# Optimization experiments

Hardware: AMD Instinct MI355X
Metric: run time of the kernel (lower is better)

The kernel has to match this reference:

```python
import jax, jax.numpy as jnp
import numpy as np

B, L, N = 2048, 64, 1024          # rows, lookback_period, nnodes
E, SE, F, NW, S = 32, 16, 8, 7, 20  # week emb, stop emb, n_features, nweekdays, stops per row
N_SHARED = E + F + SE             # 56; conv kernel width n_f = N_SHARED + 3 = 59


def setup_inputs() -> dict:
    key = jax.random.key(0)
    ks = jax.random.split(key, 12)
    return {
        "x": jax.random.normal(ks[0], (B, L, N), jnp.float32),
        "x_dist": jax.random.normal(ks[1], (N,), jnp.float32),
        "x_features": jax.random.normal(ks[2], (B, F), jnp.float32),
        "x_markov": jax.random.normal(ks[3], (B, N), jnp.float32),
        "stops": jax.random.randint(ks[4], (B, S), 0, N),
        "x_week": jax.random.randint(ks[5], (B,), 0, NW),
        "x_mask": jax.random.randint(ks[6], (B, N), 0, 2, jnp.int32),
        # learned parameters
        "stop_emb": jax.random.normal(ks[7], (N, SE), jnp.float32) * 0.1,
        "week_emb": jax.random.normal(ks[8], (NW, E), jnp.float32) * 0.1,
        "conv_w": jax.random.normal(ks[9], (N, N_SHARED + 3), jnp.float32) * 0.1,  # Conv1d weight [nnodes, 1, n_f] squeezed
        "conv_b": jax.random.normal(ks[10], (N,), jnp.float32) * 0.1,
        "fc1_w": jax.random.normal(ks[11], (L,), jnp.float32) * 0.1,  # Linear(L,1) weight
        "fc1_b": jnp.zeros((), jnp.float32),
    }


def reference(x, x_dist, x_features, x_markov, stops, x_week, x_mask,
              stop_emb, week_emb, conv_w, conv_b, fc1_w, fc1_b):
    # per-row sum of stop embeddings: [B, SE]
    x_embed = stop_emb[stops].sum(axis=1)
    # fc1 over lookback: out[b,n] = sum_l w[l] * x[b,l,n] + b   -> [B, N]
    out = jnp.einsum('bln,l->bn', x, fc1_w) + fc1_b
    # shared (node-independent) features, order matches torch concat: [week_emb, features, stop_emb_sum]
    shared = jnp.concatenate([week_emb[x_week], x_features, x_embed], axis=-1)  # [B, 56]
    # diagonal of strided Conv1d == per-node dot product with that node's kernel
    logits = (shared @ conv_w[:, :N_SHARED].T
              + out * conv_w[:, N_SHARED]
              + x_dist[None, :] * conv_w[:, N_SHARED + 1]
              + x_markov * conv_w[:, N_SHARED + 2]
              + conv_b)  # [B, N]
    logp = jax.nn.log_softmax(logits, axis=1)
    return jnp.where(x_mask.astype(bool), jnp.float32(-1e8), logp)
```

## Files before the change

### kernel.cpp

```cpp
#include <hip/hip_runtime.h>
#include <math.h>

#define BLOCK 256

constexpr int L = 64, N = 1024, E = 32, SE = 16, F = 8, S = 20;
constexpr int NSH = 56;
constexpr int NF  = 59;

typedef float f4 __attribute__((ext_vector_type(4)));

__global__ void prep(const float* __restrict__ x_features,
                     const int*   __restrict__ stops,
                     const int*   __restrict__ x_week,
                     const float* __restrict__ stop_emb,
                     const float* __restrict__ week_emb,
                     const float* __restrict__ conv_w,
                     const float* __restrict__ x_dist,
                     const float* __restrict__ conv_b,
                     float* __restrict__ sh_out,
                     float* __restrict__ w56,
                     float* __restrict__ w58,
                     float* __restrict__ colconst,
                     int B)
{
    const int blk = blockIdx.x;
    const int t = threadIdx.x;
    if (blk < B) {
        const int b = blk;
        if (t < E) {
            sh_out[b * NSH + t] = week_emb[x_week[b] * E + t];
        } else if (t < E + F) {
            sh_out[b * NSH + t] = x_features[b * F + (t - E)];
        } else if (t < NSH) {
            const int j = t - (E + F);
            float s = 0.f;
            #pragma unroll
            for (int k = 0; k < S; ++k)
                s += stop_emb[stops[b * S + k] * SE + j];
            sh_out[b * NSH + t] = s;
        }
    } else {
        const int n = (blk - B) * 64 + t;
        if (n < N) {
            const float* w = conv_w + (size_t)n * NF;
            w56[n] = w[NSH];
            w58[n] = w[NSH + 2];
            colconst[n] = x_dist[n] * w[NSH + 1] + conv_b[n];
        }
    }
}

__global__ __launch_bounds__(BLOCK, 2) void gemm_static(
    const float* __restrict__ shf,
    const float* __restrict__ conv_w,
    const float* __restrict__ colconst,
    float* __restrict__ statc)
{
    __shared__ float Ash[64][NSH + 1];
    __shared__ float Bsh[64][NSH + 1];

    const int n0 = blockIdx.x * 64;
    const int b0 = blockIdx.y * 64;
    const int t  = threadIdx.x;

    for (int idx = t; idx < 64 * NSH; idx += BLOCK) {
        const int r = idx / NSH, c = idx % NSH;
        Ash[r][c] = shf[(size_t)(b0 + r) * NSH + c];
        Bsh[r][c] = conv_w[(size_t)(n0 + r) * NF + c];
    }
    __syncthreads();

    const int tx = t & 15, ty = t >> 4;
    float acc[4][4];
    #pragma unroll
    for (int i = 0; i < 4; ++i)
        #pragma unroll
        for (int k = 0; k < 4; ++k) acc[i][k] = 0.f;

    #pragma unroll 8
    for (int j = 0; j < NSH; ++j) {
        float a[4], bb[4];
        #pragma unroll
        for (int i = 0; i < 4; ++i) a[i]  = Ash[ty * 4 + i][j];
        #pragma unroll
        for (int i = 0; i < 4; ++i) bb[i] = Bsh[tx * 4 + i][j];
        #pragma unroll
        for (int i = 0; i < 4; ++i)
            #pragma unroll
            for (int k = 0; k < 4; ++k)
                acc[i][k] = fmaf(a[i], bb[k], acc[i][k]);
    }

    const float4 cc = *(const float4*)&colconst[n0 + tx * 4];
    #pragma unroll
    for (int i = 0; i < 4; ++i) {
        float4 r;
        r.x = acc[i][0] + cc.x;
        r.y = acc[i][1] + cc.y;
        r.z = acc[i][2] + cc.z;
        r.w = acc[i][3] + cc.w;
        *(float4*)&statc[(size_t)(b0 + ty * 4 + i) * N + n0 + tx * 4] = r;
    }
}

__global__ __launch_bounds__(BLOCK, 4) void markov_main(
    const float* __restrict__ x,
    const float* __restrict__ statc,
    const float* __restrict__ w56,
    const float* __restrict__ w58,
    const float* __restrict__ x_markov,
    const int*   __restrict__ x_mask,
    const float* __restrict__ fc1_w,
    const float* __restrict__ fc1_b,
    float* __restrict__ out)
{
    constexpr int NWAVE = BLOCK / 64;
    __shared__ float sh_fc1[L];
    __shared__ float red_max[NWAVE];
    __shared__ float red_sum[NWAVE];

    const int b = blockIdx.x;
    const int t = threadIdx.x;

    if (t < L) sh_fc1[t] = fc1_w[t];
    __syncthreads();

    const f4* xb = (const f4*)(x + (size_t)b * L * N);
    f4 acc = (f4)(0.f);
    #pragma unroll 16
    for (int l = 0; l < L; ++l) {
        const float w = sh_fc1[l];
        const f4 v = __builtin_nontemporal_load(&xb[l * (N / 4) + t]);
        acc[0] = fmaf(w, v[0], acc[0]);
        acc[1] = fmaf(w, v[1], acc[1]);
        acc[2] = fmaf(w, v[2], acc[2]);
        acc[3] = fmaf(w, v[3], acc[3]);
    }
    const float bias = fc1_b[0];

    const float4 st = ((const float4*)(statc + (size_t)b * N))[t];
    const float4 wa = ((const float4*)w56)[t];
    const float4 wc = ((const float4*)w58)[t];
    const float4 mk = ((const float4*)(x_markov + (size_t)b * N))[t];

    float lg[4];
    lg[0] = st.x + (acc[0] + bias) * wa.x + mk.x * wc.x;
    lg[1] = st.y + (acc[1] + bias) * wa.y + mk.y * wc.y;
    lg[2] = st.z + (acc[2] + bias) * wa.z + mk.z * wc.z;
    lg[3] = st.w + (acc[3] + bias) * wa.w + mk.w * wc.w;

    float lmax = fmaxf(fmaxf(lg[0], lg[1]), fmaxf(lg[2], lg[3]));
    #pragma unroll
    for (int off = 32; off > 0; off >>= 1)
        lmax = fmaxf(lmax, __shfl_down(lmax, off, 64));
    if ((t & 63) == 0) red_max[t >> 6] = lmax;
    __syncthreads();
    float m = red_max[0];
    #pragma unroll
    for (int i = 1; i < NWAVE; ++i) m = fmaxf(m, red_max[i]);

    float se = 0.f;
    #pragma unroll
    for (int i = 0; i < 4; ++i) se += __expf(lg[i] - m);
    #pragma unroll
    for (int off = 32; off > 0; off >>= 1)
        se += __shfl_down(se, off, 64);
    if ((t & 63) == 0) red_sum[t >> 6] = se;
    __syncthreads();
    float Z = 0.f;
    #pragma unroll
    for (int i = 0; i < NWAVE; ++i) Z += red_sum[i];
    const float logZ = m + __logf(Z);

    const int4 mask = ((const int4*)(x_mask + (size_t)b * N))[t];
    f4 res;
    res[0] = mask.x ? -1e8f : (lg[0] - logZ);
    res[1] = mask.y ? -1e8f : (lg[1] - logZ);
    res[2] = mask.z ? -1e8f : (lg[2] - logZ);
    res[3] = mask.w ? -1e8f : (lg[3] - logZ);
    __builtin_nontemporal_store(res, &((f4*)(out + (size_t)b * N))[t]);
}

extern "C" void kernel_launch(void* const* d_in, const int* in_sizes, int n_in,
                              void* d_out, int out_size, void* d_ws, size_t ws_size,
                              hipStream_t stream) {
    const float* x          = (const float*)d_in[0];
    const float* x_dist     = (const float*)d_in[1];
    const float* x_features = (const float*)d_in[2];
    const float* x_markov   = (const float*)d_in[3];
    const int*   stops      = (const int*)  d_in[4];
    const int*   x_week     = (const int*)  d_in[5];
    const int*   x_mask     = (const int*)  d_in[6];
    const float* stop_emb   = (const float*)d_in[7];
    const float* week_emb   = (const float*)d_in[8];
    const float* conv_w     = (const float*)d_in[9];
    const float* conv_b     = (const float*)d_in[10];
    const float* fc1_w      = (const float*)d_in[11];
    const float* fc1_b      = (const float*)d_in[12];
    float* out = (float*)d_out;

    const int B = in_sizes[5];

    char* ws = (char*)d_ws;
    float* sh_f     = (float*)(ws);
    float* w56      = (float*)(ws + ((size_t)B * NSH * 4 + 255) / 256 * 256);
    float* w58      = w56 + N;
    float* colconst = w58 + N;
    float* statc    = (float*)((char*)colconst + ((size_t)N * 4 + 255) / 256 * 256);

    prep<<<B + N / 64, 64, 0, stream>>>(x_features, stops, x_week,
                                        stop_emb, week_emb, conv_w, x_dist, conv_b,
                                        sh_f, w56, w58, colconst, B);
    dim3 ggrid(N / 64, B / 64);
    gemm_static<<<ggrid, BLOCK, 0, stream>>>(sh_f, conv_w, colconst, statc);
    markov_main<<<B, BLOCK, 0, stream>>>(x, statc, w56, w58, x_markov, x_mask,
                                         fc1_w, fc1_b, out);
}
```

Measured before the change: 703.6 us.

## Fuse prep, static GEMM and softmax into one per-row kernel

Replaces the three-kernel pipeline (prep, tiled static GEMM writing a B×N buffer, main softmax kernel) with a single kernel per row. Each block builds the 56 shared features in LDS and computes its row's static logits directly from conv_w in registers. This removes the intermediate statc round-trip through global memory and two launches. The cost is redundant per-block recomputation and strided, uncoalesced conv_w reads across threads.

```diff
diff --git a/kernel.cpp b/kernel.cpp
--- a/kernel.cpp
+++ b/kernel.cpp
@@ -9,121 +9,63 @@
 
 typedef float f4 __attribute__((ext_vector_type(4)));
 
-__global__ void prep(const float* __restrict__ x_features,
-                     const int*   __restrict__ stops,
-                     const int*   __restrict__ x_week,
-                     const float* __restrict__ stop_emb,
-                     const float* __restrict__ week_emb,
-                     const float* __restrict__ conv_w,
-                     const float* __restrict__ x_dist,
-                     const float* __restrict__ conv_b,
-                     float* __restrict__ sh_out,
-                     float* __restrict__ w56,
-                     float* __restrict__ w58,
-                     float* __restrict__ colconst,
-                     int B)
-{
-    const int blk = blockIdx.x;
-    const int t = threadIdx.x;
-    if (blk < B) {
-        const int b = blk;
-        if (t < E) {
-            sh_out[b * NSH + t] = week_emb[x_week[b] * E + t];
-        } else if (t < E + F) {
-            sh_out[b * NSH + t] = x_features[b * F + (t - E)];
-        } else if (t < NSH) {
-            const int j = t - (E + F);
-            float s = 0.f;
-            #pragma unroll
-            for (int k = 0; k < S; ++k)
-                s += stop_emb[stops[b * S + k] * SE + j];
-            sh_out[b * NSH + t] = s;
-        }
-    } else {
-        const int n = (blk - B) * 64 + t;
-        if (n < N) {
-            const float* w = conv_w + (size_t)n * NF;
-            w56[n] = w[NSH];
-            w58[n] = w[NSH + 2];
-            colconst[n] = x_dist[n] * w[NSH + 1] + conv_b[n];
-        }
-    }
-}
-
-__global__ __launch_bounds__(BLOCK, 2) void gemm_static(
-    const float* __restrict__ shf,
+__global__ __launch_bounds__(BLOCK, 4) void fused_markov(
+    const float* __restrict__ x,
+    const float* __restrict__ x_dist,
+    const float* __restrict__ x_features,
+    const float* __restrict__ x_markov,
+    const int*   __restrict__ stops,
+    const int*   __restrict__ x_week,
+    const int*   __restrict__ x_mask,
+    const float* __restrict__ stop_emb,
+    const float* __restrict__ week_emb,
     const float* __restrict__ conv_w,
-    const float* __restrict__ colconst,
-    float* __restrict__ statc)
-{
-    __shared__ float Ash[64][NSH + 1];
-    __shared__ float Bsh[64][NSH + 1];
-
-    const int n0 = blockIdx.x * 64;
-    const int b0 = blockIdx.y * 64;
-    const int t  = threadIdx.x;
-
-    for (int idx = t; idx < 64 * NSH; idx += BLOCK) {
-        const int r = idx / NSH, c = idx % NSH;
-        Ash[r][c] = shf[(size_t)(b0 + r) * NSH + c];
-        Bsh[r][c] = conv_w[(size_t)(n0 + r) * NF + c];
-    }
-    __syncthreads();
-
-    const int tx = t & 15, ty = t >> 4;
-    float acc[4][4];
-    #pragma unroll
-    for (int i = 0; i < 4; ++i)
-        #pragma unroll
-        for (int k = 0; k < 4; ++k) acc[i][k] = 0.f;
-
-    #pragma unroll 8
-    for (int j = 0; j < NSH; ++j) {
-        float a[4], bb[4];
-        #pragma unroll
-        for (int i = 0; i < 4; ++i) a[i]  = Ash[ty * 4 + i][j];
-        #pragma unroll
-        for (int i = 0; i < 4; ++i) bb[i] = Bsh[tx * 4 + i][j];
-        #pragma unroll
-        for (int i = 0; i < 4; ++i)
-            #pragma unroll
-            for (int k = 0; k < 4; ++k)
-                acc[i][k] = fmaf(a[i], bb[k], acc[i][k]);
-    }
-
-    const float4 cc = *(const float4*)&colconst[n0 + tx * 4];
-    #pragma unroll
-    for (int i = 0; i < 4; ++i) {
-        float4 r;
-        r.x = acc[i][0] + cc.x;
-        r.y = acc[i][1] + cc.y;
-        r.z = acc[i][2] + cc.z;
-        r.w = acc[i][3] + cc.w;
-        *(float4*)&statc[(size_t)(b0 + ty * 4 + i) * N + n0 + tx * 4] = r;
-    }
-}
-
-__global__ __launch_bounds__(BLOCK, 4) void markov_main(
-    const float* __restrict__ x,
-    const float* __restrict__ statc,
-    const float* __restrict__ w56,
-    const float* __restrict__ w58,
-    const float* __restrict__ x_markov,
-    const int*   __restrict__ x_mask,
+    const float* __restrict__ conv_b,
     const float* __restrict__ fc1_w,
     const float* __restrict__ fc1_b,
     float* __restrict__ out)
 {
     constexpr int NWAVE = BLOCK / 64;
+    __shared__ float sh_shared[NSH];
     __shared__ float sh_fc1[L];
+    __shared__ int   sh_stops[S];
     __shared__ float red_max[NWAVE];
     __shared__ float red_sum[NWAVE];
 
     const int b = blockIdx.x;
     const int t = threadIdx.x;
 
-    if (t < L) sh_fc1[t] = fc1_w[t];
+    if (t < S) sh_stops[t] = stops[b * S + t];
+    if (t >= 64 && t < 64 + L) sh_fc1[t - 64] = fc1_w[t - 64];
     __syncthreads();
+
+    if (t < E) {
+        sh_shared[t] = week_emb[x_week[b] * E + t];
+    } else if (t < E + F) {
+        sh_shared[t] = x_features[b * F + (t - E)];
+    } else if (t < NSH) {
+        const int j = t - (E + F);
+        float s = 0.f;
+        #pragma unroll
+        for (int k = 0; k < S; ++k)
+            s += stop_emb[sh_stops[k] * SE + j];
+        sh_shared[t] = s;
+    }
+    __syncthreads();
+
+    float stat[4], w56r[4], w58r[4];
+    #pragma unroll
+    for (int i = 0; i < 4; ++i) {
+        const int n = 4 * t + i;
+        const float* __restrict__ w = conv_w + (size_t)n * NF;
+        float s = 0.f;
+        #pragma unroll 8
+        for (int j = 0; j < NSH; ++j)
+            s = fmaf(sh_shared[j], w[j], s);
+        w56r[i] = w[NSH];
+        w58r[i] = w[NSH + 2];
+        stat[i] = s + x_dist[n] * w[NSH + 1] + conv_b[n];
+    }
 
     const f4* xb = (const f4*)(x + (size_t)b * L * N);
     f4 acc = (f4)(0.f);
@@ -138,16 +80,13 @@
     }
     const float bias = fc1_b[0];
 
-    const float4 st = ((const float4*)(statc + (size_t)b * N))[t];
-    const float4 wa = ((const float4*)w56)[t];
-    const float4 wc = ((const float4*)w58)[t];
     const float4 mk = ((const float4*)(x_markov + (size_t)b * N))[t];
 
     float lg[4];
-    lg[0] = st.x + (acc[0] + bias) * wa.x + mk.x * wc.x;
-    lg[1] = st.y + (acc[1] + bias) * wa.y + mk.y * wc.y;
-    lg[2] = st.z + (acc[2] + bias) * wa.z + mk.z * wc.z;
-    lg[3] = st.w + (acc[3] + bias) * wa.w + mk.w * wc.w;
+    lg[0] = stat[0] + (acc[0] + bias) * w56r[0] + mk.x * w58r[0];
+    lg[1] = stat[1] + (acc[1] + bias) * w56r[1] + mk.y * w58r[1];
+    lg[2] = stat[2] + (acc[2] + bias) * w56r[2] + mk.z * w58r[2];
+    lg[3] = stat[3] + (acc[3] + bias) * w56r[3] + mk.w * w58r[3];
 
     float lmax = fmaxf(fmaxf(lg[0], lg[1]), fmaxf(lg[2], lg[3]));
     #pragma unroll
@@ -201,18 +140,10 @@
 
     const int B = in_sizes[5];
 
-    char* ws = (char*)d_ws;
-    float* sh_f     = (float*)(ws);
-    float* w56      = (float*)(ws + ((size_t)B * NSH * 4 + 255) / 256 * 256);
-    float* w58      = w56 + N;
-    float* colconst = w58 + N;
-    float* statc    = (float*)((char*)colconst + ((size_t)N * 4 + 255) / 256 * 256);
+    (void)d_ws; (void)ws_size;
 
-    prep<<<B + N / 64, 64, 0, stream>>>(x_features, stops, x_week,
-                                        stop_emb, week_emb, conv_w, x_dist, conv_b,
-                                        sh_f, w56, w58, colconst, B);
-    dim3 ggrid(N / 64, B / 64);
-    gemm_static<<<ggrid, BLOCK, 0, stream>>>(sh_f, conv_w, colconst, statc);
-    markov_main<<<B, BLOCK, 0, stream>>>(x, statc, w56, w58, x_markov, x_mask,
-                                         fc1_w, fc1_b, out);
+    fused_markov<<<B, BLOCK, 0, stream>>>(x, x_dist, x_features, x_markov,
+                                          stops, x_week, x_mask,
+                                          stop_emb, week_emb, conv_w, conv_b,
+                                          fc1_w, fc1_b, out);
 }
```

After: 751.2 us. +6.8%, slower.

## Split lookback reduction across blocks with partial sums and separate combine kernel

Applied to the files above, without the earlier changes.

The fc1 reduction over the 64-step lookback moves into its own kernel that splits L into 8 chunks, one block per (chunk, row). This raises the number of blocks and the memory-level parallelism available for streaming the 512 MB input. A second kernel sums the 8 partials and does the logits, softmax and masking. The cost is an extra 64 MB partial buffer that is written and read back, plus one more kernel launch.

```diff
diff --git a/kernel.cpp b/kernel.cpp
--- a/kernel.cpp
+++ b/kernel.cpp
@@ -6,6 +6,8 @@
 constexpr int L = 64, N = 1024, E = 32, SE = 16, F = 8, S = 20;
 constexpr int NSH = 56;
 constexpr int NF  = 59;
+constexpr int J   = 8;
+constexpr int LJ  = L / J;
 
 typedef float f4 __attribute__((ext_vector_type(4)));
 
@@ -103,38 +105,55 @@
     }
 }
 
-__global__ __launch_bounds__(BLOCK, 4) void markov_main(
+__global__ __launch_bounds__(BLOCK, 8) void einsum_split(
     const float* __restrict__ x,
+    const float* __restrict__ fc1_w,
+    float* __restrict__ partial)
+{
+    const int j = blockIdx.x;
+    const int b = blockIdx.y;
+    const int t = threadIdx.x;
+
+    const f4* xb = (const f4*)(x + ((size_t)b * L + (size_t)j * LJ) * N);
+    f4 acc = (f4)(0.f);
+    #pragma unroll
+    for (int l = 0; l < LJ; ++l) {
+        const float w = fc1_w[j * LJ + l];
+        const f4 v = __builtin_nontemporal_load(&xb[l * (N / 4) + t]);
+        acc[0] = fmaf(w, v[0], acc[0]);
+        acc[1] = fmaf(w, v[1], acc[1]);
+        acc[2] = fmaf(w, v[2], acc[2]);
+        acc[3] = fmaf(w, v[3], acc[3]);
+    }
+    ((f4*)(partial + ((size_t)b * J + j) * N))[t] = acc;
+}
+
+__global__ __launch_bounds__(BLOCK, 4) void combine(
+    const float* __restrict__ partial,
     const float* __restrict__ statc,
     const float* __restrict__ w56,
     const float* __restrict__ w58,
     const float* __restrict__ x_markov,
     const int*   __restrict__ x_mask,
-    const float* __restrict__ fc1_w,
     const float* __restrict__ fc1_b,
     float* __restrict__ out)
 {
     constexpr int NWAVE = BLOCK / 64;
-    __shared__ float sh_fc1[L];
     __shared__ float red_max[NWAVE];
     __shared__ float red_sum[NWAVE];
 
     const int b = blockIdx.x;
     const int t = threadIdx.x;
 
-    if (t < L) sh_fc1[t] = fc1_w[t];
-    __syncthreads();
-
-    const f4* xb = (const f4*)(x + (size_t)b * L * N);
+    const f4* pb = (const f4*)(partial + (size_t)b * J * N);
     f4 acc = (f4)(0.f);
-    #pragma unroll 16
-    for (int l = 0; l < L; ++l) {
-        const float w = sh_fc1[l];
-        const f4 v = __builtin_nontemporal_load(&xb[l * (N / 4) + t]);
-        acc[0] = fmaf(w, v[0], acc[0]);
-        acc[1] = fmaf(w, v[1], acc[1]);
-        acc[2] = fmaf(w, v[2], acc[2]);
-        acc[3] = fmaf(w, v[3], acc[3]);
+    #pragma unroll
+    for (int j = 0; j < J; ++j) {
+        const f4 v = pb[j * (N / 4) + t];
+        acc[0] += v[0];
+        acc[1] += v[1];
+        acc[2] += v[2];
+        acc[3] += v[3];
     }
     const float bias = fc1_b[0];
 
@@ -207,12 +226,15 @@
     float* w58      = w56 + N;
     float* colconst = w58 + N;
     float* statc    = (float*)((char*)colconst + ((size_t)N * 4 + 255) / 256 * 256);
+    float* partial  = statc + (size_t)B * N;
 
     prep<<<B + N / 64, 64, 0, stream>>>(x_features, stops, x_week,
                                         stop_emb, week_emb, conv_w, x_dist, conv_b,
                                         sh_f, w56, w58, colconst, B);
     dim3 ggrid(N / 64, B / 64);
     gemm_static<<<ggrid, BLOCK, 0, stream>>>(sh_f, conv_w, colconst, statc);
-    markov_main<<<B, BLOCK, 0, stream>>>(x, statc, w56, w58, x_markov, x_mask,
-                                         fc1_w, fc1_b, out);
-}
+    dim3 egrid(J, B);
+    einsum_split<<<egrid, BLOCK, 0, stream>>>(x, fc1_w, partial);
+    combine<<<B, BLOCK, 0, stream>>>(partial, statc, w56, w58, x_markov, x_mask,
+                                     fc1_b, out);
+}
```

Measured after the change: 727.9 us. +3.5%, slower.
